# Kernel optimization log

Hardware: AMD Instinct MI355X
Metric: run time of the kernel (lower is better)

## Reference

```python
import jax, jax.numpy as jnp
import numpy as np

B, S, HID = 2, 2048, 2048
H, KV, D = 32, 8, 64
GROUPS = H // KV
THETA = 10000.0
SCALE = D ** -0.5
NEG = -1e9


def setup_inputs() -> dict:
    key = jax.random.key(0)
    ks = jax.random.split(key, 5)
    x = jax.random.normal(ks[0], (B, S, 2 * HID), dtype=jnp.float32)
    # Linear weights stored as [in, out] (torch stores [out, in]; y = x @ W.T there)
    Wq = jax.random.normal(ks[1], (2 * HID, H * D), dtype=jnp.float32) * 0.02
    Wk = jax.random.normal(ks[2], (2 * HID, KV * D), dtype=jnp.float32) * 0.02
    Wv = jax.random.normal(ks[3], (2 * HID, KV * D), dtype=jnp.float32) * 0.02
    Wo = jax.random.normal(ks[4], (H * D, HID), dtype=jnp.float32) * 0.02
    # additive causal mask, broadcastable to [B, 1, S, S]
    causal = jnp.tril(jnp.ones((S, S), dtype=bool))
    attention_mask = jnp.where(causal, 0.0, NEG)[None, None].astype(jnp.float32)
    position_ids = jnp.broadcast_to(jnp.arange(S, dtype=jnp.int32)[None, :], (B, S))
    return {"combined_states": x, "attention_mask": attention_mask,
            "position_ids": position_ids, "Wq": Wq, "Wk": Wk, "Wv": Wv, "Wo": Wo}


def _rotate_half(x):
    x1, x2 = jnp.split(x, 2, axis=-1)
    return jnp.concatenate([-x2, x1], axis=-1)


def _rope_cos_sin(position_ids, dtype):
    inv_freq = 1.0 / (THETA ** (jnp.arange(0, D, 2, dtype=jnp.float32) / D))  # [D/2]
    freqs = position_ids.astype(jnp.float32)[..., None] * inv_freq  # [B, S, D/2]
    emb = jnp.concatenate([freqs, freqs], axis=-1)  # [B, S, D]
    return jnp.cos(emb).astype(dtype), jnp.sin(emb).astype(dtype)


def reference(combined_states, attention_mask, position_ids, Wq, Wk, Wv, Wo):
    x = combined_states
    q = (x @ Wq).reshape(B, S, H, D).transpose(0, 2, 1, 3)    # [B, H, S, D]
    k = (x @ Wk).reshape(B, S, KV, D).transpose(0, 2, 1, 3)   # [B, KV, S, D]
    v = (x @ Wv).reshape(B, S, KV, D).transpose(0, 2, 1, 3)
    cos, sin = _rope_cos_sin(position_ids, x.dtype)           # [B, S, D]
    cos, sin = cos[:, None], sin[:, None]                     # [B, 1, S, D]
    q = q * cos + _rotate_half(q) * sin
    k = k * cos + _rotate_half(k) * sin
    k = jnp.repeat(k, GROUPS, axis=1)                         # [B, H, S, D]
    v = jnp.repeat(v, GROUPS, axis=1)
    scores = jnp.einsum('bhqd,bhkd->bhqk', q, k) * SCALE + attention_mask
    probs = jax.nn.softmax(scores.astype(jnp.float32), axis=-1).astype(q.dtype)
    attn = jnp.einsum('bhqk,bhkd->bhqd', probs, v)            # [B, H, S, D]
    attn = attn.transpose(0, 2, 1, 3).reshape(B, S, H * D)
    return attn @ Wo
```

## Files before the change

kernel.cpp:

```cpp
#include <hip/hip_runtime.h>

#define S_LEN 2048
#define BATCH 2
#define HEADS 32
#define KVH   8
#define DH    64

typedef unsigned short u16;
typedef unsigned int   u32;
typedef u16   u16x8 __attribute__((ext_vector_type(8)));
typedef u16   u16x4 __attribute__((ext_vector_type(4)));
typedef short s16x8 __attribute__((ext_vector_type(8)));
typedef float f32x4 __attribute__((ext_vector_type(4)));
typedef u32   u32x2 __attribute__((ext_vector_type(2)));

__device__ __forceinline__ u16 f2bf(float f) {
    unsigned x; __builtin_memcpy(&x, &f, 4);
    x += 0x7fffu + ((x >> 16) & 1u);
    return (u16)(x >> 16);
}
__device__ __forceinline__ float bf2f(u16 u) {
    unsigned x = ((unsigned)u) << 16; float f; __builtin_memcpy(&f, &x, 4); return f;
}
__device__ __forceinline__ float fexp2(float x) {
#if __has_builtin(__builtin_amdgcn_exp2f)
    return __builtin_amdgcn_exp2f(x);
#else
    return exp2f(x);
#endif
}
__device__ __forceinline__ void gll16(const void* g, void* l) {
    __builtin_amdgcn_global_load_lds((const __attribute__((address_space(1))) unsigned*)g,
                                     (__attribute__((address_space(3))) unsigned*)l, 16, 0, 0);
}

__global__ __launch_bounds__(256) void k_f32_to_bf16(const float* __restrict__ src,
                                                     u16* __restrict__ dst, int n4) {
    int i = blockIdx.x * 256 + threadIdx.x;
    if (i < n4) {
        f32x4 v = ((const f32x4*)src)[i];
        u16x4 o;
        o.x = f2bf(v.x); o.y = f2bf(v.y); o.z = f2bf(v.z); o.w = f2bf(v.w);
        ((u16x4*)dst)[i] = o;
    }
}

__global__ __launch_bounds__(256) void k_wprep(const float* __restrict__ Wq, const float* __restrict__ Wk,
                                               const float* __restrict__ Wv, const float* __restrict__ Wo,
                                               u16* __restrict__ wqkvt, u16* __restrict__ wot) {
    __shared__ float t[32][33];
    int id = blockIdx.x;
    const float* src; u16* dst; int srcCols, dstStride, dstRowOff, bx, by;
    if (id < 8192)       { src = Wq; dst = wqkvt; srcCols = 2048; dstStride = 4096; dstRowOff = 0;    bx = id & 127; by = id >> 7; }
    else if (id < 10240) { id -= 8192;  src = Wk; dst = wqkvt; srcCols = 512; dstStride = 4096; dstRowOff = 2048; bx = id & 127; by = id >> 7; }
    else if (id < 12288) { id -= 10240; src = Wv; dst = wqkvt; srcCols = 512; dstStride = 4096; dstRowOff = 2560; bx = id & 127; by = id >> 7; }
    else                 { id -= 12288; src = Wo; dst = wot;   srcCols = 2048; dstStride = 2048; dstRowOff = 0;   bx = id & 63;  by = id >> 6; }
    int r0 = bx * 32, c0 = by * 32;
    int tx = threadIdx.x & 31, ty = threadIdx.x >> 5;
#pragma unroll
    for (int i = 0; i < 4; ++i)
        t[ty + 8 * i][tx] = src[(size_t)(r0 + ty + 8 * i) * srcCols + (c0 + tx)];
    __syncthreads();
#pragma unroll
    for (int i = 0; i < 4; ++i)
        dst[(size_t)(dstRowOff + c0 + ty + 8 * i) * dstStride + (r0 + tx)] = f2bf(t[tx][ty + 8 * i]);
}

template <int OUT_BF16>
__global__ __launch_bounds__(256) void k_gemm_bt(const u16* __restrict__ A,
                                                 const u16* __restrict__ Bt,
                                                 void* __restrict__ Cout,
                                                 int M, int N, int K) {
    __shared__ __align__(16) u16 As[8192];
    __shared__ __align__(16) u16 Bs[8192];
    int tid = threadIdx.x;
    int wave = tid >> 6, lane = tid & 63, m15 = lane & 15, quad = lane >> 4;
    int wm = (wave >> 1) * 64, wn = (wave & 1) * 64;

    int nwg = gridDim.x * gridDim.y;
    int bid = blockIdx.y * gridDim.x + blockIdx.x;
    if ((nwg & 7) == 0) bid = (bid & 7) * (nwg >> 3) + (bid >> 3);
    int bx = bid % gridDim.x, by = bid / gridDim.x;
    int m0 = by * 128, n0 = bx * 128;

    f32x4 acc[4][4];
#pragma unroll
    for (int i = 0; i < 4; ++i)
#pragma unroll
        for (int j = 0; j < 4; ++j) acc[i][j] = (f32x4){0.f, 0.f, 0.f, 0.f};

    int rl8 = lane >> 3;
    int sg8 = ((lane & 7) ^ rl8) * 8;
    const u16* Ag = A  + (size_t)(m0 + wave * 32 + rl8) * K + sg8;
    const u16* Bg = Bt + (size_t)(n0 + wave * 32 + rl8) * K + sg8;
    u16* Asl = As + (wave * 32) * 64;
    u16* Bsl = Bs + (wave * 32) * 64;
    int swq = m15 & 7;

    for (int k0 = 0; k0 < K; k0 += 64) {
        __syncthreads();
#pragma unroll
        for (int i = 0; i < 4; ++i) {
            gll16(Ag + (size_t)(8 * i) * K, Asl + (8 * i) * 64);
            gll16(Bg + (size_t)(8 * i) * K, Bsl + (8 * i) * 64);
        }
        Ag += 64; Bg += 64;
        __syncthreads();

#pragma unroll
        for (int kk = 0; kk < 2; ++kk) {
            int sgr = ((kk * 4 + quad) ^ swq) * 8;
            s16x8 af[4], bfr[4];
#pragma unroll
            for (int mt = 0; mt < 4; ++mt)
                af[mt] = *(const s16x8*)&As[(wm + mt * 16 + m15) * 64 + sgr];
#pragma unroll
            for (int nt = 0; nt < 4; ++nt)
                bfr[nt] = *(const s16x8*)&Bs[(wn + nt * 16 + m15) * 64 + sgr];
#pragma unroll
            for (int mt = 0; mt < 4; ++mt)
#pragma unroll
                for (int nt = 0; nt < 4; ++nt)
                    acc[mt][nt] = __builtin_amdgcn_mfma_f32_16x16x32_bf16(af[mt], bfr[nt], acc[mt][nt], 0, 0, 0);
        }
    }

#pragma unroll
    for (int mt = 0; mt < 4; ++mt)
#pragma unroll
        for (int nt = 0; nt < 4; ++nt)
#pragma unroll
            for (int r = 0; r < 4; ++r) {
                size_t row = m0 + wm + mt * 16 + quad * 4 + r;
                size_t col = n0 + wn + nt * 16 + m15;
                float v = acc[mt][nt][r];
                if (OUT_BF16) ((u16*)Cout)[row * N + col] = f2bf(v);
                else          ((float*)Cout)[row * N + col] = v;
            }
}

__global__ __launch_bounds__(512, 2) void k_gemm8p(const u16* __restrict__ A,
                                                   const u16* __restrict__ Bt,
                                                   u16* __restrict__ Cout,
                                                   int M, int N, int K) {
    __shared__ __align__(16) u16 Ls[8][8192];
    const int tid = threadIdx.x;
    const int wave = tid >> 6, lane = tid & 63;
    const int m15 = lane & 15, quad = lane >> 4;
    const int wm = wave >> 2, wn = wave & 3;
    const int rl8 = lane >> 3;
    const int sg8 = ((lane & 7) ^ rl8) * 8;
    const int m0 = blockIdx.y * 256, n0 = blockIdx.x * 256;

    const u16* Abase = A  + (size_t)(m0 + wave * 16 + rl8) * K + sg8;
    const u16* Bbase = Bt + (size_t)(n0 + wave * 16 + rl8) * K + sg8;
    u16* Lst = &Ls[0][0] + wave * 1024;
    const int aro = (wm * 16 + m15) * 64;
    const int bro = (wn * 16 + m15) * 64;
    const int sx = m15 & 7;

    f32x4 acc[8][4];
#pragma unroll
    for (int i = 0; i < 8; ++i)
#pragma unroll
        for (int j = 0; j < 4; ++j) acc[i][j] = (f32x4){0.f, 0.f, 0.f, 0.f};
    s16x8 rA0[8], rA1[8], rB0[4], rB1[4];

#define STG8(slot, c, t) do { \
    const u16* gsrc_ = ((c) & 1) ? Abase : Bbase; \
    size_t off_ = (size_t)(((c) >> 1) * 128) * K + (size_t)(t) * 64; \
    u16* ld_ = Lst + (slot) * 8192; \
    gll16(gsrc_ + off_, ld_); \
    gll16(gsrc_ + off_ + (size_t)8 * K, ld_ + 512); \
} while (0)

#define RDA8(slot, rg) do { \
    const u16* sb_ = &Ls[slot][0] + aro; \
    _Pragma("unroll") \
    for (int mt_ = 0; mt_ < 4; ++mt_) \
        _Pragma("unroll") \
        for (int kk_ = 0; kk_ < 2; ++kk_) \
            rg[mt_ * 2 + kk_] = *(const s16x8*)&sb_[mt_ * 2048 + (((kk_ * 4 + quad) ^ sx) * 8)]; \
} while (0)

#define RDB8(slot, rg) do { \
    const u16* sb_ = &Ls[slot][0] + bro; \
    _Pragma("unroll") \
    for (int nt_ = 0; nt_ < 2; ++nt_) \
        _Pragma("unroll") \
        for (int kk_ = 0; kk_ < 2; ++kk_) \
            rg[nt_ * 2 + kk_] = *(const s16x8*)&sb_[nt_ * 4096 + (((kk_ * 4 + quad) ^ sx) * 8)]; \
} while (0)

#define MM8(ra, rb, mi, ni) do { \
    _Pragma("unroll") \
    for (int mt_ = 0; mt_ < 4; ++mt_) \
        _Pragma("unroll") \
        for (int nt_ = 0; nt_ < 2; ++nt_) \
            _Pragma("unroll") \
            for (int kk_ = 0; kk_ < 2; ++kk_) \
                acc[(mi) + mt_][(ni) + nt_] = __builtin_amdgcn_mfma_f32_16x16x32_bf16( \
                    ra[mt_ * 2 + kk_], rb[nt_ * 2 + kk_], acc[(mi) + mt_][(ni) + nt_], 0, 0, 0); \
} while (0)

#define BAR8() asm volatile("s_barrier" ::: "memory")
#define LGKM8() do { asm volatile("s_waitcnt lgkmcnt(0)" ::: "memory"); \
                     __builtin_amdgcn_sched_barrier(0); } while (0)
#define GUARD8(more) do { \
    if (more) asm volatile("s_waitcnt vmcnt(6)" ::: "memory"); \
    else      asm volatile("s_waitcnt vmcnt(0)" ::: "memory"); \
} while (0)

    const int NT2 = K >> 7;

    STG8(0, 0, 0); STG8(1, 1, 0); STG8(2, 2, 0); STG8(3, 3, 0);
    STG8(4, 0, 1); STG8(5, 1, 1); STG8(6, 2, 1);
    asm volatile("s_waitcnt vmcnt(6)" ::: "memory");
    BAR8();

    for (int it = 0; it < NT2; ++it) {
        const int t2 = 2 * it + 2, t3 = 2 * it + 3;
        const bool more = (it < NT2 - 1);

        RDB8(0, rB0);
        STG8(7, 3, 2 * it + 1);
        BAR8(); LGKM8();
        if (it) {
            __builtin_amdgcn_s_setprio(1);
            MM8(rA1, rB1, 4, 2);
            __builtin_amdgcn_s_setprio(0);
        }
        BAR8();
        RDA8(1, rA0);
        if (more) STG8(0, 0, t2);
        BAR8(); LGKM8();
        __builtin_amdgcn_s_setprio(1);
        MM8(rA0, rB0, 0, 0);
        __builtin_amdgcn_s_setprio(0);
        BAR8();
        RDB8(2, rB1);
        if (more) STG8(1, 1, t2);
        BAR8(); LGKM8();
        __builtin_amdgcn_s_setprio(1);
        MM8(rA0, rB1, 0, 2);
        __builtin_amdgcn_s_setprio(0);
        BAR8();
        RDA8(3, rA1);
        if (more) STG8(2, 2, t2);
        BAR8(); LGKM8();
        __builtin_amdgcn_s_setprio(1);
        MM8(rA1, rB0, 4, 0);
        __builtin_amdgcn_s_setprio(0);
        GUARD8(more);
        BAR8();
        RDB8(4, rB0);
        if (more) STG8(3, 3, t2);
        BAR8(); LGKM8();
        __builtin_amdgcn_s_setprio(1);
        MM8(rA1, rB1, 4, 2);
        __builtin_amdgcn_s_setprio(0);
        BAR8();
        RDA8(5, rA0);
        if (more) STG8(4, 0, t3);
        BAR8(); LGKM8();
        __builtin_amdgcn_s_setprio(1);
        MM8(rA0, rB0, 0, 0);
        __builtin_amdgcn_s_setprio(0);
        BAR8();
        RDB8(6, rB1);
        if (more) STG8(5, 1, t3);
        BAR8(); LGKM8();
        __builtin_amdgcn_s_setprio(1);
        MM8(rA0, rB1, 0, 2);
        __builtin_amdgcn_s_setprio(0);
        BAR8();
        RDA8(7, rA1);
        if (more) STG8(6, 2, t3);
        BAR8(); LGKM8();
        __builtin_amdgcn_s_setprio(1);
        MM8(rA1, rB0, 4, 0);
        __builtin_amdgcn_s_setprio(0);
        GUARD8(more);
        BAR8();
    }
    MM8(rA1, rB1, 4, 2);

#pragma unroll
    for (int i = 0; i < 8; ++i) {
        size_t row = (size_t)(m0 + (i & 3) * 32 + wm * 16 + (i >> 2) * 128 + quad * 4);
#pragma unroll
        for (int j = 0; j < 4; ++j) {
            size_t col = (size_t)(n0 + (j & 1) * 64 + wn * 16 + (j >> 1) * 128 + m15);
#pragma unroll
            for (int r = 0; r < 4; ++r)
                Cout[(row + r) * N + col] = f2bf(acc[i][j][r]);
        }
    }
#undef STG8
#undef RDA8
#undef RDB8
#undef MM8
#undef BAR8
#undef LGKM8
#undef GUARD8
}

__global__ __launch_bounds__(256) void k_vtrans(const u16* __restrict__ qkv, u16* __restrict__ vt) {
    __shared__ u16 t[64][72];
    int s0 = blockIdx.x * 64;
    int bkv = blockIdx.y;
    int tid = threadIdx.x;
    int row = tid >> 2, seg = tid & 3;
    int b = bkv >> 3, kv = bkv & 7;
    const u16* src = qkv + (size_t)(b * S_LEN + s0 + row) * 3072 + 2560 + kv * 64 + seg * 16;
    *(u16x8*)&t[row][seg * 16]     = *(const u16x8*)(src);
    *(u16x8*)&t[row][seg * 16 + 8] = *(const u16x8*)(src + 8);
    __syncthreads();
    int d = tid >> 2, sseg = tid & 3;
    u16x8 o0, o1;
#pragma unroll
    for (int j = 0; j < 8; ++j) {
        o0[j] = t[(j & 3) * 16 + sseg * 4 + (j >> 2)][d];
        o1[j] = t[(j & 3) * 16 + sseg * 4 + (j >> 2) + 2][d];
    }
    u16* dst = vt + ((size_t)bkv * 64 + d) * S_LEN + s0 + sseg * 16;
    *(u16x8*)(dst)     = o0;
    *(u16x8*)(dst + 8) = o1;
}

__global__ __launch_bounds__(256) void k_rope(const u16* __restrict__ qkv,
                                              const int* __restrict__ pos_ids,
                                              u16* __restrict__ qo, u16* __restrict__ ko) {
    int bs = blockIdx.x;
    int b = bs >> 11, s = bs & 2047;
    int tid = threadIdx.x;
    float pos = (float)pos_ids[bs];
    const u16* row = qkv + (size_t)bs * 3072;

#pragma unroll
    for (int p = tid; p < 1024; p += 256) {
        int h = p >> 5, i = p & 31;
        float inv = fexp2((float)i * -0.4152410119f);
        float ang = pos * inv;
        float sn, c; __sincosf(ang, &sn, &c);
        float a = bf2f(row[h * 64 + i]);
        float bq = bf2f(row[h * 64 + i + 32]);
        size_t base = ((size_t)(b * HEADS + h) * S_LEN + s) * DH;
        qo[base + i]      = f2bf(a * c - bq * sn);
        qo[base + i + 32] = f2bf(bq * c + a * sn);
    }
    {
        int p = tid;
        if (p < 256) {
            int kv = p >> 5, i = p & 31;
            float inv = fexp2((float)i * -0.4152410119f);
            float ang = pos * inv;
            float sn, c; __sincosf(ang, &sn, &c);
            float a = bf2f(row[2048 + kv * 64 + i]);
            float bk = bf2f(row[2048 + kv * 64 + i + 32]);
            size_t base = ((size_t)(b * KVH + kv) * S_LEN + s) * DH;
            ko[base + i]      = f2bf(a * c - bk * sn);
            ko[base + i + 32] = f2bf(bk * c + a * sn);
        }
    }
}

__global__ __launch_bounds__(256) void k_attn(const u16* __restrict__ q, const u16* __restrict__ k,
                                              const u16* __restrict__ vt, u16* __restrict__ out) {
    __shared__ __align__(16) u16 Qs[4096];
    __shared__ __align__(16) u16 Ks[8192];
    __shared__ __align__(16) u16 Vts[8192];
    __shared__ __align__(16) u16 Ps[4 * 16 * 72];
    int bh = blockIdx.y;
    int b = bh >> 5, h = bh & 31, kvh = h >> 2;
    int tid = threadIdx.x, wave = tid >> 6, lane = tid & 63, m15 = lane & 15, quad = lane >> 4;

    const u16* qhb = q + (size_t)(b * HEADS + h) * S_LEN * DH;
    const u16* kb  = k + (size_t)(b * KVH + kvh) * S_LEN * DH;
    const u16* vb  = vt + (size_t)(b * KVH + kvh) * DH * S_LEN;
    u16* PsW = &Ps[wave * 16 * 72];
    const float C = 0.1803368801f;

    int rl8 = lane >> 3;
    int sg8 = ((lane & 7) ^ rl8) * 8;
    int swq = m15 & 7;
    int vrow = lane >> 4;
    int vgrp = lane & 15;

    for (int half = 0; half < 2; ++half) {
        int jt = half ? (31 - (int)blockIdx.x) : (int)blockIdx.x;
        int q0 = jt * 64;
        __syncthreads();
        {
            const u16* qg = qhb + (size_t)(q0 + wave * 16 + rl8) * DH + sg8;
            gll16(qg,          Qs + (wave * 16) * 64);
            gll16(qg + 8 * DH, Qs + (wave * 16 + 8) * 64);
        }

        float lsum[4];
        f32x4 oacc[4];
#pragma unroll
        for (int r = 0; r < 4; ++r) lsum[r] = 0.f;
#pragma unroll
        for (int dt = 0; dt < 4; ++dt) oacc[dt] = (f32x4){0.f, 0.f, 0.f, 0.f};

        for (int ib = 0; ib <= jt; ib += 2) {
            int kk0 = ib * 64;
            int nsub = (jt - ib >= 1) ? 2 : 1;
            __syncthreads();
            {
                const u16* kg = kb + (size_t)(kk0 + wave * 32 + rl8) * DH + sg8;
#pragma unroll
                for (int i = 0; i < 4; ++i)
                    gll16(kg + (size_t)(8 * i) * DH, Ks + (wave * 32 + 8 * i) * 64);
#pragma unroll
                for (int i = 0; i < 4; ++i) {
                    int d = wave * 16 + 4 * i + vrow;
                    const u16* vg = vb + (size_t)d * S_LEN + kk0 + ((vgrp ^ (d & 7)) * 8);
                    gll16(vg, Vts + (wave * 16 + 4 * i) * 128);
                }
            }
            __syncthreads();

            for (int sub = 0; sub < nsub; ++sub) {
                f32x4 sacc[4];
#pragma unroll
                for (int nt = 0; nt < 4; ++nt) sacc[nt] = (f32x4){0.f, 0.f, 0.f, 0.f};
#pragma unroll
                for (int kk = 0; kk < 2; ++kk) {
                    int sgr = ((kk * 4 + quad) ^ swq) * 8;
                    s16x8 aF = *(const s16x8*)&Qs[(wave * 16 + m15) * 64 + sgr];
#pragma unroll
                    for (int nt = 0; nt < 4; ++nt) {
                        s16x8 bF = *(const s16x8*)&Ks[(sub * 64 + nt * 16 + m15) * 64 + sgr];
                        sacc[nt] = __builtin_amdgcn_mfma_f32_16x16x32_bf16(aF, bF, sacc[nt], 0, 0, 0);
                    }
                }

                bool dsub = (kk0 + sub * 64) == q0;
#pragma unroll
                for (int r = 0; r < 4; ++r) {
                    int qrr = wave * 16 + quad * 4 + r;
                    float p0[4];
#pragma unroll
                    for (int nt = 0; nt < 4; ++nt) {
                        float s2 = sacc[nt][r] * C - 12.0f;
                        if (dsub && (nt * 16 + m15 > qrr)) s2 = -1e30f;
                        p0[nt] = fexp2(s2);
                        lsum[r] += p0[nt];
                    }
                    unsigned a0, a1, a2, a3;
                    __builtin_memcpy(&a0, &p0[0], 4); __builtin_memcpy(&a1, &p0[1], 4);
                    __builtin_memcpy(&a2, &p0[2], 4); __builtin_memcpy(&a3, &p0[3], 4);
                    u32x2 w;
                    w.x = (a0 >> 16) | (a1 & 0xffff0000u);
                    w.y = (a2 >> 16) | (a3 & 0xffff0000u);
                    *(u32x2*)&PsW[(quad * 4 + r) * 72 + m15 * 4] = w;
                }

#pragma unroll
                for (int kk = 0; kk < 2; ++kk) {
                    s16x8 aF = *(const s16x8*)&PsW[m15 * 72 + kk * 32 + quad * 8];
                    int g = (sub * 8 + kk * 4 + quad) ^ swq;
#pragma unroll
                    for (int dt = 0; dt < 4; ++dt) {
                        s16x8 bF = *(const s16x8*)&Vts[(dt * 16 + m15) * 128 + g * 8];
                        oacc[dt] = __builtin_amdgcn_mfma_f32_16x16x32_bf16(aF, bF, oacc[dt], 0, 0, 0);
                    }
                }
            }
        }

#pragma unroll
        for (int r = 0; r < 4; ++r) {
            float ls = lsum[r];
#pragma unroll
            for (int off = 1; off < 16; off <<= 1) ls += __shfl_xor(ls, off, 64);
            float inv = 1.f / ls;
            int qrow = q0 + wave * 16 + quad * 4 + r;
#pragma unroll
            for (int dt = 0; dt < 4; ++dt)
                out[((size_t)(b * S_LEN) + qrow) * (size_t)(HEADS * DH) + h * DH + dt * 16 + m15] =
                    f2bf(oacc[dt][r] * inv);
        }
    }
}

extern "C" void kernel_launch(void* const* d_in, const int* in_sizes, int n_in,
                              void* d_out, int out_size, void* d_ws, size_t ws_size,
                              hipStream_t stream) {
    const float* x  = (const float*)d_in[0];
    const int*   pos = (const int*)d_in[2];
    const float* Wq = (const float*)d_in[3];
    const float* Wk = (const float*)d_in[4];
    const float* Wv = (const float*)d_in[5];
    const float* Wo = (const float*)d_in[6];

    char* ws = (char*)d_ws;
    const size_t NEED = 92274688;
    if (ws_size < NEED) return;

    u16* xbf   = (u16*)(ws);
    u16* vt    = (u16*)(ws + 16777216);
    u16* wqkvt = (u16*)(ws + 33554432);
    u16* wot   = (u16*)(ws + 58720256);
    u16* qkv   = (u16*)(ws + 67108864);
    u16* qro   = wqkvt;
    u16* kro   = qro + 8388608;
    u16* attn  = xbf;

    k_f32_to_bf16<<<16384, 256, 0, stream>>>(x, xbf, 4194304);
    k_wprep<<<16384, 256, 0, stream>>>(Wq, Wk, Wv, Wo, wqkvt, wot);
    { dim3 g(12, 16); k_gemm8p<<<g, 512, 0, stream>>>(xbf, wqkvt, qkv, 4096, 3072, 4096); }
    { dim3 g(32, 16); k_vtrans<<<g, 256, 0, stream>>>(qkv, vt); }
    k_rope<<<4096, 256, 0, stream>>>(qkv, pos, qro, kro);
    { dim3 g(16, 64); k_attn<<<g, 256, 0, stream>>>(qro, kro, vt, attn); }
    { dim3 g(16, 32); k_gemm_bt<0><<<g, 256, 0, stream>>>(attn, wot, (float*)d_out, 4096, 2048, 2048); }
}
```

Baseline: 404.3 us.

## Overlap LDS fragment reads with MFMA via double-buffered register fragments in GEMM

Each LDS read of the next A/B fragment now sits in the same phase as the MFMA block instead of after a barrier. The A/B register fragments are duplicated (a/b sets) so reads can target fresh registers while the MFMAs consume the old ones. The first B read moves out of the loop. This is meant to hide LDS latency and cut barrier-separated phases, at the cost of more VGPRs, which may lower occupancy or cause spills. The reordering of GUARD8 around barriers also changes the sync pattern, which needs to stay correct against the async global-to-LDS stages.

```diff
diff --git a/kernel.cpp b/kernel.cpp
--- a/kernel.cpp
+++ b/kernel.cpp
@@ -164,7 +164,8 @@
     for (int i = 0; i < 8; ++i)
 #pragma unroll
         for (int j = 0; j < 4; ++j) acc[i][j] = (f32x4){0.f, 0.f, 0.f, 0.f};
-    s16x8 rA0[8], rA1[8], rB0[4], rB1[4];
+    s16x8 rA0a[8], rA1a[8], rA0b[8], rA1b[8];
+    s16x8 rB0a[4], rB1a[4], rB0b[4], rB1b[4];
 
 #define STG8(slot, c, t) do { \
     const u16* gsrc_ = ((c) & 1) ? Abase : Bbase; \
@@ -217,73 +218,72 @@
     STG8(4, 0, 1); STG8(5, 1, 1); STG8(6, 2, 1);
     asm volatile("s_waitcnt vmcnt(6)" ::: "memory");
     BAR8();
+    RDB8(0, rB0a);
 
     for (int it = 0; it < NT2; ++it) {
         const int t2 = 2 * it + 2, t3 = 2 * it + 3;
         const bool more = (it < NT2 - 1);
 
-        RDB8(0, rB0);
         STG8(7, 3, 2 * it + 1);
         BAR8(); LGKM8();
-        if (it) {
-            __builtin_amdgcn_s_setprio(1);
-            MM8(rA1, rB1, 4, 2);
-            __builtin_amdgcn_s_setprio(0);
-        }
-        BAR8();
-        RDA8(1, rA0);
+        __builtin_amdgcn_s_setprio(1);
+        if (it) MM8(rA1b, rB1b, 4, 2);
+        RDA8(1, rA0a);
+        __builtin_amdgcn_s_setprio(0);
+        BAR8();
         if (more) STG8(0, 0, t2);
         BAR8(); LGKM8();
         __builtin_amdgcn_s_setprio(1);
-        MM8(rA0, rB0, 0, 0);
-        __builtin_amdgcn_s_setprio(0);
-        BAR8();
-        RDB8(2, rB1);
+        MM8(rA0a, rB0a, 0, 0);
+        RDB8(2, rB1a);
+        __builtin_amdgcn_s_setprio(0);
+        BAR8();
         if (more) STG8(1, 1, t2);
         BAR8(); LGKM8();
         __builtin_amdgcn_s_setprio(1);
-        MM8(rA0, rB1, 0, 2);
-        __builtin_amdgcn_s_setprio(0);
-        BAR8();
-        RDA8(3, rA1);
+        MM8(rA0a, rB1a, 0, 2);
+        RDA8(3, rA1a);
+        __builtin_amdgcn_s_setprio(0);
+        BAR8();
         if (more) STG8(2, 2, t2);
         BAR8(); LGKM8();
-        __builtin_amdgcn_s_setprio(1);
-        MM8(rA1, rB0, 4, 0);
-        __builtin_amdgcn_s_setprio(0);
         GUARD8(more);
-        BAR8();
-        RDB8(4, rB0);
+        __builtin_amdgcn_s_setprio(1);
+        MM8(rA1a, rB0a, 4, 0);
+        RDB8(4, rB0b);
+        __builtin_amdgcn_s_setprio(0);
+        BAR8();
         if (more) STG8(3, 3, t2);
         BAR8(); LGKM8();
         __builtin_amdgcn_s_setprio(1);
-        MM8(rA1, rB1, 4, 2);
-        __builtin_amdgcn_s_setprio(0);
-        BAR8();
-        RDA8(5, rA0);
+        MM8(rA1a, rB1a, 4, 2);
+        RDA8(5, rA0b);
+        __builtin_amdgcn_s_setprio(0);
+        BAR8();
         if (more) STG8(4, 0, t3);
         BAR8(); LGKM8();
         __builtin_amdgcn_s_setprio(1);
-        MM8(rA0, rB0, 0, 0);
-        __builtin_amdgcn_s_setprio(0);
-        BAR8();
-        RDB8(6, rB1);
+        MM8(rA0b, rB0b, 0, 0);
+        RDB8(6, rB1b);
+        __builtin_amdgcn_s_setprio(0);
+        BAR8();
         if (more) STG8(5, 1, t3);
         BAR8(); LGKM8();
         __builtin_amdgcn_s_setprio(1);
-        MM8(rA0, rB1, 0, 2);
-        __builtin_amdgcn_s_setprio(0);
-        BAR8();
-        RDA8(7, rA1);
+        MM8(rA0b, rB1b, 0, 2);
+        RDA8(7, rA1b);
+        __builtin_amdgcn_s_setprio(0);
+        BAR8();
         if (more) STG8(6, 2, t3);
         BAR8(); LGKM8();
-        __builtin_amdgcn_s_setprio(1);
-        MM8(rA1, rB0, 4, 0);
-        __builtin_amdgcn_s_setprio(0);
         GUARD8(more);
-        BAR8();
-    }
-    MM8(rA1, rB1, 4, 2);
+        __builtin_amdgcn_s_setprio(1);
+        MM8(rA1b, rB0b, 4, 0);
+        if (more) RDB8(0, rB0a);
+        __builtin_amdgcn_s_setprio(0);
+        BAR8();
+    }
+    MM8(rA1b, rB1b, 4, 2);
 
 #pragma unroll
     for (int i = 0; i < 8; ++i) {
```

New measurement: 399.2 us. About the same (-1.3%).
